# Optimization experiments

Measured on AMD Instinct MI355X. Metric: run time of the kernel, lower is better.

## Reference

```python
import jax, jax.numpy as jnp
import numpy as np

B, S_PREV, E, H, LOW = 8, 4095, 2048, 16, 512
HD = E // H  # 128
ROPE_BASE = 10000.0


def _rope(x, pos):
    # x: [..., S, d], pos: [S]; half-split rotary
    d = x.shape[-1]
    half = d // 2
    inv_freq = 1.0 / (ROPE_BASE ** (jnp.arange(half, dtype=jnp.float32) / half))
    ang = pos.astype(jnp.float32)[:, None] * inv_freq  # [S, half]
    cos, sin = jnp.cos(ang), jnp.sin(ang)
    x1, x2 = x[..., :half], x[..., half:]
    return jnp.concatenate([x1 * cos - x2 * sin, x1 * sin + x2 * cos], axis=-1)


def setup_inputs() -> dict:
    key = jax.random.key(0)
    ks = jax.random.split(key, 10)

    def w(k, *shape):
        return jax.random.normal(k, shape, dtype=jnp.float32) * (1.0 / np.float32(np.sqrt(shape[0])))

    return {
        "x": jax.random.normal(ks[0], (B, 1, E), dtype=jnp.float32),
        "ckv_cache": jax.random.normal(ks[1], (B, S_PREV, LOW), dtype=jnp.float32),
        "kr_cache": jax.random.normal(ks[2], (B, S_PREV, HD), dtype=jnp.float32),
        "Wdq": w(ks[3], E, E),
        "Wuq": w(ks[4], E, E),
        "Wqr": w(ks[5], E, HD),
        "Wdkv": w(ks[6], E, LOW),
        "Wkr": w(ks[7], E, HD),
        "fused_upsample": w(ks[8], LOW, 2 * E),
        "Wo": w(ks[9], E, E),
    }


def reference(x, ckv_cache, kr_cache, Wdq, Wuq, Wqr, Wdkv, Wkr, fused_upsample, Wo):
    Bx = x.shape[0]
    # update compressed KV caches with the current token
    ckv = jnp.concatenate([ckv_cache, x @ Wdkv], axis=1)            # [B,S,LOW]
    kr = jnp.concatenate([kr_cache, x @ Wkr], axis=1)               # [B,S,HD]
    S = ckv.shape[1]
    up = ckv @ fused_upsample                                       # [B,S,2E]
    k_up, v = up[..., :E], up[..., E:]
    Kc = k_up.reshape(Bx, S, H, HD).transpose(0, 2, 1, 3)           # [B,H,S,HD]
    Kr = _rope(kr, jnp.arange(S))                                   # [B,S,HD] shared rope-K
    Kr = jnp.broadcast_to(Kr[:, None], (Bx, H, S, HD))
    v = v.reshape(Bx, S, H, HD).transpose(0, 2, 1, 3)               # [B,H,S,HD]
    # query path
    Cq = x @ Wdq                                                    # [B,1,E]
    Qc = (Cq @ Wuq).reshape(Bx, 1, H, HD).transpose(0, 2, 1, 3)     # [B,H,1,HD]
    Qr = _rope(Cq @ Wqr, jnp.arange(S - 1, S))                      # [B,1,HD] at last pos
    Qr = jnp.broadcast_to(Qr[:, None], (Bx, H, 1, HD))
    q = jnp.concatenate([Qc, Qr], axis=-1)                          # [B,H,1,2HD]
    k = jnp.concatenate([Kc, Kr], axis=-1)                          # [B,H,S,2HD]
    scores = jnp.einsum('bhqd,bhkd->bhqk', q, k) / np.float32(np.sqrt(2 * HD))
    attn = jax.nn.softmax(scores, axis=-1)
    o = jnp.einsum('bhqk,bhkd->bhqd', attn, v)                      # [B,H,1,HD]
    out = o.transpose(0, 2, 1, 3).reshape(Bx, 1, E) @ Wo            # [B,1,E]
    return out
```

## Files before the change

kernel.cpp:

```cpp
#include <hip/hip_runtime.h>
#include <hip/hip_bf16.h>

#define B_ 8
#define SPREV 4095
#define S_ 4096
#define E_ 2048
#define H_ 16
#define HD_ 128
#define LOW_ 512
#define NCH 64
#define CHK 64

typedef short s8v __attribute__((ext_vector_type(8)));
typedef float f4v __attribute__((ext_vector_type(4)));

__device__ __forceinline__ short f2bf_s(float f) {
  return (short)__bfloat16_as_ushort(__float2bfloat16(f));
}
__device__ __forceinline__ float bf2f(unsigned short h) {
  union { unsigned u; float f; } v; v.u = ((unsigned)h) << 16;
  return v.f;
}

__global__ __launch_bounds__(256) void init_kernel(float* __restrict__ ws_pre,
                                                   float* __restrict__ out,
                                                   float2* __restrict__ tab2) {
  int i = blockIdx.x * 256 + threadIdx.x;
  if (i < 120832) ws_pre[i] = 0.f;
  else if (i < 137216) out[i - 120832] = 0.f;
  int s = i >> 6, j = i & 63;
  float invf = powf(10000.0f, -(float)j * (1.0f / 64.0f));
  float sn, cs; sincosf((float)s * invf, &sn, &cs);
  tab2[i] = make_float2(cs, sn);
}

__global__ __launch_bounds__(128) void matvec8(
    const float* __restrict__ x, int K,
    const float* __restrict__ W0, int N0, float* __restrict__ o0,
    const float* __restrict__ W1, int N1, float* __restrict__ o1,
    const float* __restrict__ W2, int N2, float* __restrict__ o2)
{
  int cb = blockIdx.x;
  int nb0 = N0 >> 7, nb1 = N1 >> 7;
  const float* W; float* o; int N, colbase;
  if (cb < nb0)            { W = W0; o = o0; N = N0; colbase = cb << 7; }
  else if (cb < nb0 + nb1) { W = W1; o = o1; N = N1; colbase = (cb - nb0) << 7; }
  else                     { W = W2; o = o2; N = N2; colbase = (cb - nb0 - nb1) << 7; }
  int col = colbase + threadIdx.x;
  int k0 = blockIdx.y * 32;
  float acc[B_];
  #pragma unroll
  for (int b = 0; b < B_; ++b) acc[b] = 0.f;
  const float* Wp = W + (size_t)k0 * N + col;
  #pragma unroll 8
  for (int k = 0; k < 32; ++k) {
    float wv = Wp[(size_t)k * N];
    #pragma unroll
    for (int b = 0; b < B_; ++b)
      acc[b] = fmaf(x[b * K + k0 + k], wv, acc[b]);
  }
  #pragma unroll
  for (int b = 0; b < B_; ++b) atomicAdd(&o[b * N + col], acc[b]);
}

__global__ __launch_bounds__(256) void qeff_rope_kernel(
    const float* __restrict__ Qc, const float* __restrict__ FU,
    unsigned short* __restrict__ qeff,
    const float* __restrict__ kr_cache, const float* __restrict__ kr_new,
    const float* __restrict__ qr_pre, const float2* __restrict__ tab2,
    float* __restrict__ score_r)
{
  int bx = blockIdx.x, b = blockIdx.y, t = threadIdx.x;
  int g = t >> 4, li = t & 15;
  if (bx < 16) {
    int h = bx;
    __shared__ float qs[HD_];
    if (t < 128) qs[t] = Qc[b * E_ + h * HD_ + t];
    __syncthreads();
    f4v q0 = *(const f4v*)&qs[li * 8];
    f4v q1 = *(const f4v*)&qs[li * 8 + 4];
    #pragma unroll 4
    for (int p = 0; p < 32; ++p) {
      int l = p * 16 + g;
      const f4v* w4 = (const f4v*)(FU + (size_t)l * (2 * E_) + h * HD_ + li * 8);
      f4v w0 = w4[0], w1 = w4[1];
      float a = w0[0]*q0[0] + w0[1]*q0[1] + w0[2]*q0[2] + w0[3]*q0[3]
              + w1[0]*q1[0] + w1[1]*q1[1] + w1[2]*q1[2] + w1[3]*q1[3];
      a += __shfl_xor(a, 1); a += __shfl_xor(a, 2);
      a += __shfl_xor(a, 4); a += __shfl_xor(a, 8);
      if (li == 0) qeff[(size_t)(b * H_ + h) * LOW_ + l] = (unsigned short)f2bf_s(a);
    }
  } else {
    int s_base = (bx - 16) * 256;
    __shared__ float qr[128];
    if (t < 64) {
      float invf = powf(10000.0f, -(float)t * (1.0f / 64.0f));
      float x1 = qr_pre[b * HD_ + t], x2 = qr_pre[b * HD_ + 64 + t];
      float sn, cs; sincosf(4095.0f * invf, &sn, &cs);
      qr[t]      = x1 * cs - x2 * sn;
      qr[64 + t] = x1 * sn + x2 * cs;
    }
    __syncthreads();
    f4v qa = *(const f4v*)&qr[li * 4];
    f4v qb = *(const f4v*)&qr[64 + li * 4];
    #pragma unroll 2
    for (int p = 0; p < 16; ++p) {
      int s = s_base + p * 16 + g;
      const float* krp = (s == S_ - 1) ? (kr_new + b * HD_)
                                       : (kr_cache + ((size_t)b * SPREV + s) * HD_);
      f4v x1 = *(const f4v*)&krp[li * 4];
      f4v x2 = *(const f4v*)&krp[64 + li * 4];
      const float2* tp = &tab2[(size_t)s * 64 + li * 4];
      float dot = 0.f;
      #pragma unroll
      for (int q = 0; q < 4; ++q) {
        float2 cs2 = tp[q];
        dot += qa[q] * (x1[q] * cs2.x - x2[q] * cs2.y)
             + qb[q] * (x1[q] * cs2.y + x2[q] * cs2.x);
      }
      dot += __shfl_xor(dot, 1); dot += __shfl_xor(dot, 2);
      dot += __shfl_xor(dot, 4); dot += __shfl_xor(dot, 8);
      if (li == 0) score_r[b * S_ + s] = dot;
    }
  }
}

__global__ __launch_bounds__(256) void attn_kernel(
    const float* __restrict__ ckv_cache, const float* __restrict__ ckv_new,
    const unsigned short* __restrict__ qeff, const float* __restrict__ score_r,
    unsigned short* __restrict__ acc_part, float* __restrict__ m_part,
    float* __restrict__ l_part)
{
  int chunk = blockIdx.x, b = blockIdx.y;
  int tid = threadIdx.x;
  int w = tid >> 6, lane = tid & 63;
  int kg = lane >> 4, l16 = lane & 15;
  __shared__ float S_lds[16 * 64];
  __shared__ unsigned short P_lds[16 * 64];

  {
    int s_loc = w * 16 + l16;
    int s = chunk * CHK + s_loc;
    const float* crow = (s == S_ - 1) ? (ckv_new + b * LOW_)
                                      : (ckv_cache + ((size_t)b * SPREV + s) * LOW_);
    f4v acc = {0.f, 0.f, 0.f, 0.f};
    const s8v* qf = (const s8v*)(qeff + (size_t)(b * H_ + l16) * LOW_);
    #pragma unroll
    for (int kt = 0; kt < 16; ++kt) {
      s8v a = qf[kt * 4 + kg];
      const float* cp = crow + kt * 32 + kg * 8;
      f4v c0 = *(const f4v*)cp;
      f4v c1 = *(const f4v*)(cp + 4);
      s8v bv;
      bv[0]=f2bf_s(c0[0]); bv[1]=f2bf_s(c0[1]); bv[2]=f2bf_s(c0[2]); bv[3]=f2bf_s(c0[3]);
      bv[4]=f2bf_s(c1[0]); bv[5]=f2bf_s(c1[1]); bv[6]=f2bf_s(c1[2]); bv[7]=f2bf_s(c1[3]);
      acc = __builtin_amdgcn_mfma_f32_16x16x32_bf16(a, bv, acc, 0, 0, 0);
    }
    #pragma unroll
    for (int r = 0; r < 4; ++r) {
      int h = kg * 4 + r;
      S_lds[h * 64 + (s_loc ^ ((h & 7) << 2))] = acc[r];
    }
  }
  __syncthreads();

  if (w == 0) {
    int h = l16, part = kg;
    float v[16];
    #pragma unroll
    for (int jj = 0; jj < 4; ++jj) {
      int sb = part * 16 + jj * 4;
      f4v sv = *(const f4v*)&S_lds[h * 64 + (sb ^ ((h & 7) << 2))];
      f4v rv = *(const f4v*)&score_r[b * S_ + chunk * CHK + sb];
      #pragma unroll
      for (int q = 0; q < 4; ++q) v[jj * 4 + q] = (sv[q] + rv[q]) * 0.0625f;
    }
    float m = v[0];
    #pragma unroll
    for (int j = 1; j < 16; ++j) m = fmaxf(m, v[j]);
    m = fmaxf(m, __shfl_xor(m, 16));
    m = fmaxf(m, __shfl_xor(m, 32));
    float lsum = 0.f;
    #pragma unroll
    for (int j = 0; j < 16; ++j) { v[j] = expf(v[j] - m); lsum += v[j]; }
    lsum += __shfl_xor(lsum, 16);
    lsum += __shfl_xor(lsum, 32);
    #pragma unroll
    for (int jj = 0; jj < 8; ++jj) {
      int sb = part * 16 + jj * 2;
      unsigned pk = (unsigned)(unsigned short)f2bf_s(v[jj*2]) |
                    ((unsigned)(unsigned short)f2bf_s(v[jj*2+1]) << 16);
      *(unsigned*)&P_lds[h * 64 + (sb ^ ((h & 7) << 3))] = pk;
    }
    if (part == 0) {
      int idx = (b * NCH + chunk) * H_ + h;
      m_part[idx] = m;
      l_part[idx] = lsum;
    }
  }
  __syncthreads();

  {
    s8v pa[2];
    const float* rp[2][8];
    #pragma unroll
    for (int kt = 0; kt < 2; ++kt) {
      int so = kt * 32 + kg * 8;
      pa[kt] = *(const s8v*)&P_lds[l16 * 64 + (so ^ ((l16 & 7) << 3))];
      #pragma unroll
      for (int i = 0; i < 8; ++i) {
        int s = chunk * CHK + so + i;
        rp[kt][i] = (s == S_ - 1) ? (ckv_new + b * LOW_)
                                  : (ckv_cache + ((size_t)b * SPREV + s) * LOW_);
      }
    }
    f4v oa[8];
    #pragma unroll
    for (int nt = 0; nt < 8; ++nt) oa[nt] = {0.f, 0.f, 0.f, 0.f};
    #pragma unroll
    for (int nt = 0; nt < 8; ++nt) {
      int l = w * 128 + nt * 16 + l16;
      #pragma unroll
      for (int kt = 0; kt < 2; ++kt) {
        s8v bv;
        #pragma unroll
        for (int i = 0; i < 8; ++i) bv[i] = (short)f2bf_s(rp[kt][i][l]);
        oa[nt] = __builtin_amdgcn_mfma_f32_16x16x32_bf16(pa[kt], bv, oa[nt], 0, 0, 0);
      }
    }
    size_t base = (size_t)(b * NCH + chunk) * H_;
    #pragma unroll
    for (int nt = 0; nt < 8; ++nt) {
      int l = w * 128 + nt * 16 + l16;
      #pragma unroll
      for (int r = 0; r < 4; ++r) {
        int h = kg * 4 + r;
        acc_part[(base + h) * LOW_ + l] = (unsigned short)f2bf_s(oa[nt][r]);
      }
    }
  }
}

__global__ __launch_bounds__(128) void reduce_kernel(
    const float* __restrict__ m_part, const float* __restrict__ l_part,
    const unsigned short* __restrict__ acc_part, float* __restrict__ wl)
{
  int h = blockIdx.x, b = blockIdx.y, cz = blockIdx.z, t = threadIdx.x;
  __shared__ float wli[8];
  if (t < 64) {
    float mc = m_part[(b * NCH + t) * H_ + h];
    float M = mc;
    #pragma unroll
    for (int d = 1; d < 64; d <<= 1) M = fmaxf(M, __shfl_xor(M, d));
    float wc = expf(mc - M);
    float L = l_part[(b * NCH + t) * H_ + h] * wc;
    #pragma unroll
    for (int d = 1; d < 64; d <<= 1) L += __shfl_xor(L, d);
    int rel = t - cz * 8;
    if (rel >= 0 && rel < 8) wli[rel] = wc / L;
  }
  __syncthreads();
  int l0 = t * 4;
  float a0 = 0.f, a1 = 0.f, a2 = 0.f, a3 = 0.f;
  const unsigned short* ap =
      acc_part + ((size_t)(b * NCH + cz * 8) * H_ + h) * LOW_ + l0;
  #pragma unroll
  for (int c = 0; c < 8; ++c) {
    uint2 pk = *(const uint2*)(ap + (size_t)c * H_ * LOW_);
    float wc = wli[c];
    a0 = fmaf(bf2f((unsigned short)(pk.x & 0xffffu)), wc, a0);
    a1 = fmaf(bf2f((unsigned short)(pk.x >> 16)),     wc, a1);
    a2 = fmaf(bf2f((unsigned short)(pk.y & 0xffffu)), wc, a2);
    a3 = fmaf(bf2f((unsigned short)(pk.y >> 16)),     wc, a3);
  }
  float* wp = wl + (size_t)(b * H_ + h) * LOW_ + l0;
  atomicAdd(wp, a0); atomicAdd(wp + 1, a1);
  atomicAdd(wp + 2, a2); atomicAdd(wp + 3, a3);
}

__global__ __launch_bounds__(128) void proj_kernel(
    const float* __restrict__ wl, const float* __restrict__ FU,
    float* __restrict__ o_heads)
{
  int h = blockIdx.x, b = blockIdx.y, lz = blockIdx.z, d = threadIdx.x;
  __shared__ float wsh[64];
  if (d < 64) wsh[d] = wl[(b * H_ + h) * LOW_ + lz * 64 + d];
  __syncthreads();
  float a = 0.f;
  const float* fp = FU + (size_t)(lz * 64) * (2 * E_) + E_ + h * HD_ + d;
  #pragma unroll 4
  for (int l = 0; l < 64; ++l)
    a = fmaf(wsh[l], fp[(size_t)l * (2 * E_)], a);
  atomicAdd(&o_heads[(b * H_ + h) * HD_ + d], a);
}

extern "C" void kernel_launch(void* const* d_in, const int* in_sizes, int n_in,
                              void* d_out, int out_size, void* d_ws, size_t ws_size,
                              hipStream_t stream)
{
  const float* x    = (const float*)d_in[0];
  const float* ckvc = (const float*)d_in[1];
  const float* krc  = (const float*)d_in[2];
  const float* Wdq  = (const float*)d_in[3];
  const float* Wuq  = (const float*)d_in[4];
  const float* Wqr  = (const float*)d_in[5];
  const float* Wdkv = (const float*)d_in[6];
  const float* Wkr  = (const float*)d_in[7];
  const float* FU   = (const float*)d_in[8];
  const float* Wo   = (const float*)d_in[9];
  float* out = (float*)d_out;

  char* ws = (char*)d_ws;
  float* Cq             = (float*)(ws + 0);
  float* Qc             = (float*)(ws + 65536);
  float* qr_pre         = (float*)(ws + 131072);
  float* ckvn           = (float*)(ws + 135168);
  float* krn            = (float*)(ws + 151552);
  float* wl             = (float*)(ws + 155648);
  float* o_heads        = (float*)(ws + 417792);
  unsigned short* qeff  = (unsigned short*)(ws + 483328);
  float* score_r        = (float*)(ws + 614400);
  float* m_part         = (float*)(ws + 745472);
  float* l_part         = (float*)(ws + 778240);
  unsigned short* accp  = (unsigned short*)(ws + 811008);
  float2* tab2          = (float2*)(ws + 9199616);

  init_kernel<<<1024, 256, 0, stream>>>((float*)ws, out, tab2);

  matvec8<<<dim3(21, 64), 128, 0, stream>>>(x, E_, Wdq, E_, Cq,
                                            Wdkv, LOW_, ckvn, Wkr, HD_, krn);
  matvec8<<<dim3(17, 64), 128, 0, stream>>>(Cq, E_, Wuq, E_, Qc,
                                            Wqr, HD_, qr_pre,
                                            (const float*)nullptr, 0, (float*)nullptr);
  qeff_rope_kernel<<<dim3(32, 8), 256, 0, stream>>>(Qc, FU, qeff,
                                                    krc, krn, qr_pre, tab2, score_r);
  attn_kernel<<<dim3(64, 8), 256, 0, stream>>>(ckvc, ckvn, qeff, score_r,
                                               accp, m_part, l_part);
  reduce_kernel<<<dim3(16, 8, 8), 128, 0, stream>>>(m_part, l_part, accp, wl);
  proj_kernel<<<dim3(16, 8, 8), 128, 0, stream>>>(wl, FU, o_heads);
  matvec8<<<dim3(16, 64), 128, 0, stream>>>(o_heads, E_, Wo, E_, out,
                                            (const float*)nullptr, 0, (float*)nullptr,
                                            (const float*)nullptr, 0, (float*)nullptr);
}
```

Measured before the change: 96.76 us.

## Fuse rope scoring into attention and merge reduce with projection kernel

The rope-K score computation moves from the qeff kernel into the attention kernel, where each block computes the rotary dot products for its own 64 positions into LDS, so the score_r global buffer goes away. The qeff kernel is split across 4x more blocks to raise parallelism. The partial-softmax reduce and the value up-projection are merged into one kernel, which drops the wl intermediate, its atomics and one launch. In exchange, each projection block now redoes the combine over all 64 chunks for its slice, and the attention kernel does more work per block.

```diff
diff --git a/kernel.cpp b/kernel.cpp
--- a/kernel.cpp
+++ b/kernel.cpp
@@ -26,8 +26,8 @@
                                                    float* __restrict__ out,
                                                    float2* __restrict__ tab2) {
   int i = blockIdx.x * 256 + threadIdx.x;
-  if (i < 120832) ws_pre[i] = 0.f;
-  else if (i < 137216) out[i - 120832] = 0.f;
+  if (i < 55296) ws_pre[i] = 0.f;
+  else if (i < 71680) out[i - 55296] = 0.f;
   int s = i >> 6, j = i & 63;
   float invf = powf(10000.0f, -(float)j * (1.0f / 64.0f));
   float sn, cs; sincosf((float)s * invf, &sn, &cs);
@@ -63,71 +63,36 @@
   for (int b = 0; b < B_; ++b) atomicAdd(&o[b * N + col], acc[b]);
 }
 
-__global__ __launch_bounds__(256) void qeff_rope_kernel(
+__global__ __launch_bounds__(256) void qeff_kernel(
     const float* __restrict__ Qc, const float* __restrict__ FU,
-    unsigned short* __restrict__ qeff,
+    unsigned short* __restrict__ qeff)
+{
+  int bx = blockIdx.x, b = blockIdx.y, t = threadIdx.x;
+  int h = bx >> 2, lq = bx & 3;
+  int g = t >> 4, li = t & 15;
+  __shared__ float qs[HD_];
+  if (t < 128) qs[t] = Qc[b * E_ + h * HD_ + t];
+  __syncthreads();
+  f4v q0 = *(const f4v*)&qs[li * 8];
+  f4v q1 = *(const f4v*)&qs[li * 8 + 4];
+  #pragma unroll 2
+  for (int p = 0; p < 8; ++p) {
+    int l = lq * 128 + p * 16 + g;
+    const f4v* w4 = (const f4v*)(FU + (size_t)l * (2 * E_) + h * HD_ + li * 8);
+    f4v w0 = w4[0], w1 = w4[1];
+    float a = w0[0]*q0[0] + w0[1]*q0[1] + w0[2]*q0[2] + w0[3]*q0[3]
+            + w1[0]*q1[0] + w1[1]*q1[1] + w1[2]*q1[2] + w1[3]*q1[3];
+    a += __shfl_xor(a, 1); a += __shfl_xor(a, 2);
+    a += __shfl_xor(a, 4); a += __shfl_xor(a, 8);
+    if (li == 0) qeff[(size_t)(b * H_ + h) * LOW_ + l] = (unsigned short)f2bf_s(a);
+  }
+}
+
+__global__ __launch_bounds__(256) void attn_kernel(
+    const float* __restrict__ ckv_cache, const float* __restrict__ ckv_new,
+    const unsigned short* __restrict__ qeff,
     const float* __restrict__ kr_cache, const float* __restrict__ kr_new,
     const float* __restrict__ qr_pre, const float2* __restrict__ tab2,
-    float* __restrict__ score_r)
-{
-  int bx = blockIdx.x, b = blockIdx.y, t = threadIdx.x;
-  int g = t >> 4, li = t & 15;
-  if (bx < 16) {
-    int h = bx;
-    __shared__ float qs[HD_];
-    if (t < 128) qs[t] = Qc[b * E_ + h * HD_ + t];
-    __syncthreads();
-    f4v q0 = *(const f4v*)&qs[li * 8];
-    f4v q1 = *(const f4v*)&qs[li * 8 + 4];
-    #pragma unroll 4
-    for (int p = 0; p < 32; ++p) {
-      int l = p * 16 + g;
-      const f4v* w4 = (const f4v*)(FU + (size_t)l * (2 * E_) + h * HD_ + li * 8);
-      f4v w0 = w4[0], w1 = w4[1];
-      float a = w0[0]*q0[0] + w0[1]*q0[1] + w0[2]*q0[2] + w0[3]*q0[3]
-              + w1[0]*q1[0] + w1[1]*q1[1] + w1[2]*q1[2] + w1[3]*q1[3];
-      a += __shfl_xor(a, 1); a += __shfl_xor(a, 2);
-      a += __shfl_xor(a, 4); a += __shfl_xor(a, 8);
-      if (li == 0) qeff[(size_t)(b * H_ + h) * LOW_ + l] = (unsigned short)f2bf_s(a);
-    }
-  } else {
-    int s_base = (bx - 16) * 256;
-    __shared__ float qr[128];
-    if (t < 64) {
-      float invf = powf(10000.0f, -(float)t * (1.0f / 64.0f));
-      float x1 = qr_pre[b * HD_ + t], x2 = qr_pre[b * HD_ + 64 + t];
-      float sn, cs; sincosf(4095.0f * invf, &sn, &cs);
-      qr[t]      = x1 * cs - x2 * sn;
-      qr[64 + t] = x1 * sn + x2 * cs;
-    }
-    __syncthreads();
-    f4v qa = *(const f4v*)&qr[li * 4];
-    f4v qb = *(const f4v*)&qr[64 + li * 4];
-    #pragma unroll 2
-    for (int p = 0; p < 16; ++p) {
-      int s = s_base + p * 16 + g;
-      const float* krp = (s == S_ - 1) ? (kr_new + b * HD_)
-                                       : (kr_cache + ((size_t)b * SPREV + s) * HD_);
-      f4v x1 = *(const f4v*)&krp[li * 4];
-      f4v x2 = *(const f4v*)&krp[64 + li * 4];
-      const float2* tp = &tab2[(size_t)s * 64 + li * 4];
-      float dot = 0.f;
-      #pragma unroll
-      for (int q = 0; q < 4; ++q) {
-        float2 cs2 = tp[q];
-        dot += qa[q] * (x1[q] * cs2.x - x2[q] * cs2.y)
-             + qb[q] * (x1[q] * cs2.y + x2[q] * cs2.x);
-      }
-      dot += __shfl_xor(dot, 1); dot += __shfl_xor(dot, 2);
-      dot += __shfl_xor(dot, 4); dot += __shfl_xor(dot, 8);
-      if (li == 0) score_r[b * S_ + s] = dot;
-    }
-  }
-}
-
-__global__ __launch_bounds__(256) void attn_kernel(
-    const float* __restrict__ ckv_cache, const float* __restrict__ ckv_new,
-    const unsigned short* __restrict__ qeff, const float* __restrict__ score_r,
     unsigned short* __restrict__ acc_part, float* __restrict__ m_part,
     float* __restrict__ l_part)
 {
@@ -137,6 +102,17 @@
   int kg = lane >> 4, l16 = lane & 15;
   __shared__ float S_lds[16 * 64];
   __shared__ unsigned short P_lds[16 * 64];
+  __shared__ float qr_sh[128];
+  __shared__ float rope_lds[64];
+
+  if (tid < 64) {
+    float invf = powf(10000.0f, -(float)tid * (1.0f / 64.0f));
+    float x1 = qr_pre[b * HD_ + tid], x2 = qr_pre[b * HD_ + 64 + tid];
+    float sn, cs; sincosf(4095.0f * invf, &sn, &cs);
+    qr_sh[tid]      = x1 * cs - x2 * sn;
+    qr_sh[64 + tid] = x1 * sn + x2 * cs;
+  }
+  __syncthreads();
 
   {
     int s_loc = w * 16 + l16;
@@ -161,6 +137,27 @@
       int h = kg * 4 + r;
       S_lds[h * 64 + (s_loc ^ ((h & 7) << 2))] = acc[r];
     }
+    const float* krp = (s == S_ - 1) ? (kr_new + b * HD_)
+                                     : (kr_cache + ((size_t)b * SPREV + s) * HD_);
+    float rdot = 0.f;
+    #pragma unroll
+    for (int q = 0; q < 4; ++q) {
+      int j = kg * 16 + q * 4;
+      f4v x1 = *(const f4v*)&krp[j];
+      f4v x2 = *(const f4v*)&krp[64 + j];
+      f4v qa = *(const f4v*)&qr_sh[j];
+      f4v qb = *(const f4v*)&qr_sh[64 + j];
+      const float2* tp = &tab2[(size_t)s * 64 + j];
+      #pragma unroll
+      for (int k = 0; k < 4; ++k) {
+        float2 cs2 = tp[k];
+        rdot += qa[k] * (x1[k] * cs2.x - x2[k] * cs2.y)
+              + qb[k] * (x1[k] * cs2.y + x2[k] * cs2.x);
+      }
+    }
+    rdot += __shfl_xor(rdot, 16);
+    rdot += __shfl_xor(rdot, 32);
+    if (kg == 0) rope_lds[s_loc] = rdot;
   }
   __syncthreads();
 
@@ -171,7 +168,7 @@
     for (int jj = 0; jj < 4; ++jj) {
       int sb = part * 16 + jj * 4;
       f4v sv = *(const f4v*)&S_lds[h * 64 + (sb ^ ((h & 7) << 2))];
-      f4v rv = *(const f4v*)&score_r[b * S_ + chunk * CHK + sb];
+      f4v rv = *(const f4v*)&rope_lds[sb];
       #pragma unroll
       for (int q = 0; q < 4; ++q) v[jj * 4 + q] = (sv[q] + rv[q]) * 0.0625f;
     }
@@ -241,12 +238,16 @@
   }
 }
 
-__global__ __launch_bounds__(128) void reduce_kernel(
+__global__ __launch_bounds__(128) void reduce_proj_kernel(
     const float* __restrict__ m_part, const float* __restrict__ l_part,
-    const unsigned short* __restrict__ acc_part, float* __restrict__ wl)
-{
-  int h = blockIdx.x, b = blockIdx.y, cz = blockIdx.z, t = threadIdx.x;
-  __shared__ float wli[8];
+    const unsigned short* __restrict__ acc_part, const float* __restrict__ FU,
+    float* __restrict__ o_heads)
+{
+  int h = blockIdx.x, b = blockIdx.y, lz = blockIdx.z, t = threadIdx.x;
+  __shared__ float wls[NCH];
+  __shared__ float Linv_s;
+  __shared__ float pa0[128], pa1[128];
+  __shared__ float wl_sh[64];
   if (t < 64) {
     float mc = m_part[(b * NCH + t) * H_ + h];
     float M = mc;
@@ -256,42 +257,42 @@
     float L = l_part[(b * NCH + t) * H_ + h] * wc;
     #pragma unroll
     for (int d = 1; d < 64; d <<= 1) L += __shfl_xor(L, d);
-    int rel = t - cz * 8;
-    if (rel >= 0 && rel < 8) wli[rel] = wc / L;
-  }
-  __syncthreads();
-  int l0 = t * 4;
-  float a0 = 0.f, a1 = 0.f, a2 = 0.f, a3 = 0.f;
-  const unsigned short* ap =
-      acc_part + ((size_t)(b * NCH + cz * 8) * H_ + h) * LOW_ + l0;
-  #pragma unroll
-  for (int c = 0; c < 8; ++c) {
-    uint2 pk = *(const uint2*)(ap + (size_t)c * H_ * LOW_);
-    float wc = wli[c];
-    a0 = fmaf(bf2f((unsigned short)(pk.x & 0xffffu)), wc, a0);
-    a1 = fmaf(bf2f((unsigned short)(pk.x >> 16)),     wc, a1);
-    a2 = fmaf(bf2f((unsigned short)(pk.y & 0xffffu)), wc, a2);
-    a3 = fmaf(bf2f((unsigned short)(pk.y >> 16)),     wc, a3);
-  }
-  float* wp = wl + (size_t)(b * H_ + h) * LOW_ + l0;
-  atomicAdd(wp, a0); atomicAdd(wp + 1, a1);
-  atomicAdd(wp + 2, a2); atomicAdd(wp + 3, a3);
-}
-
-__global__ __launch_bounds__(128) void proj_kernel(
-    const float* __restrict__ wl, const float* __restrict__ FU,
-    float* __restrict__ o_heads)
-{
-  int h = blockIdx.x, b = blockIdx.y, lz = blockIdx.z, d = threadIdx.x;
-  __shared__ float wsh[64];
-  if (d < 64) wsh[d] = wl[(b * H_ + h) * LOW_ + lz * 64 + d];
-  __syncthreads();
-  float a = 0.f;
-  const float* fp = FU + (size_t)(lz * 64) * (2 * E_) + E_ + h * HD_ + d;
-  #pragma unroll 4
-  for (int l = 0; l < 64; ++l)
-    a = fmaf(wsh[l], fp[(size_t)l * (2 * E_)], a);
-  atomicAdd(&o_heads[(b * H_ + h) * HD_ + d], a);
+    wls[t] = wc;
+    if (t == 0) Linv_s = 1.0f / L;
+  }
+  __syncthreads();
+  {
+    int p = t & 31, ch = t >> 5;
+    int l0 = lz * 64 + p * 2;
+    float a0 = 0.f, a1 = 0.f;
+    const unsigned short* ap =
+        acc_part + ((size_t)(b * NCH + ch * 16) * H_ + h) * LOW_ + l0;
+    #pragma unroll 4
+    for (int c = 0; c < 16; ++c) {
+      unsigned pk = *(const unsigned*)(ap + (size_t)c * H_ * LOW_);
+      float wc = wls[ch * 16 + c];
+      a0 = fmaf(bf2f((unsigned short)(pk & 0xffffu)), wc, a0);
+      a1 = fmaf(bf2f((unsigned short)(pk >> 16)),     wc, a1);
+    }
+    pa0[t] = a0; pa1[t] = a1;
+  }
+  __syncthreads();
+  if (t < 32) {
+    float inv = Linv_s;
+    float s0 = pa0[t] + pa0[t + 32] + pa0[t + 64] + pa0[t + 96];
+    float s1 = pa1[t] + pa1[t + 32] + pa1[t + 64] + pa1[t + 96];
+    wl_sh[t * 2]     = s0 * inv;
+    wl_sh[t * 2 + 1] = s1 * inv;
+  }
+  __syncthreads();
+  {
+    float a = 0.f;
+    const float* fp = FU + (size_t)(lz * 64) * (2 * E_) + E_ + h * HD_ + t;
+    #pragma unroll 4
+    for (int l = 0; l < 64; ++l)
+      a = fmaf(wl_sh[l], fp[(size_t)l * (2 * E_)], a);
+    atomicAdd(&o_heads[(b * H_ + h) * HD_ + t], a);
+  }
 }
 
 extern "C" void kernel_launch(void* const* d_in, const int* in_sizes, int n_in,
@@ -316,14 +317,12 @@
   float* qr_pre         = (float*)(ws + 131072);
   float* ckvn           = (float*)(ws + 135168);
   float* krn            = (float*)(ws + 151552);
-  float* wl             = (float*)(ws + 155648);
-  float* o_heads        = (float*)(ws + 417792);
-  unsigned short* qeff  = (unsigned short*)(ws + 483328);
-  float* score_r        = (float*)(ws + 614400);
-  float* m_part         = (float*)(ws + 745472);
-  float* l_part         = (float*)(ws + 778240);
-  unsigned short* accp  = (unsigned short*)(ws + 811008);
-  float2* tab2          = (float2*)(ws + 9199616);
+  float* o_heads        = (float*)(ws + 155648);
+  unsigned short* qeff  = (unsigned short*)(ws + 221184);
+  float* m_part         = (float*)(ws + 352256);
+  float* l_part         = (float*)(ws + 385024);
+  unsigned short* accp  = (unsigned short*)(ws + 417792);
+  float2* tab2          = (float2*)(ws + 8806400);
 
   init_kernel<<<1024, 256, 0, stream>>>((float*)ws, out, tab2);
 
@@ -332,12 +331,11 @@
   matvec8<<<dim3(17, 64), 128, 0, stream>>>(Cq, E_, Wuq, E_, Qc,
                                             Wqr, HD_, qr_pre,
                                             (const float*)nullptr, 0, (float*)nullptr);
-  qeff_rope_kernel<<<dim3(32, 8), 256, 0, stream>>>(Qc, FU, qeff,
-                                                    krc, krn, qr_pre, tab2, score_r);
-  attn_kernel<<<dim3(64, 8), 256, 0, stream>>>(ckvc, ckvn, qeff, score_r,
-                                               accp, m_part, l_part);
-  reduce_kernel<<<dim3(16, 8, 8), 128, 0, stream>>>(m_part, l_part, accp, wl);
-  proj_kernel<<<dim3(16, 8, 8), 128, 0, stream>>>(wl, FU, o_heads);
+  qeff_kernel<<<dim3(64, 8), 256, 0, stream>>>(Qc, FU, qeff);
+  attn_kernel<<<dim3(64, 8), 256, 0, stream>>>(ckvc, ckvn, qeff, krc, krn,
+                                               qr_pre, tab2, accp, m_part, l_part);
+  reduce_proj_kernel<<<dim3(16, 8, 8), 128, 0, stream>>>(m_part, l_part, accp,
+                                                         FU, o_heads);
   matvec8<<<dim3(16, 64), 128, 0, stream>>>(o_heads, E_, Wo, E_, out,
                                             (const float*)nullptr, 0, (float*)nullptr,
                                             (const float*)nullptr, 0, (float*)nullptr);
```

New measurement: 83.98 us. 1.15x faster.
